# Performance work log

Hardware: AMD Instinct MI355X
Metric: run time of the kernel (lower is better)

## Reference

```python
import jax, jax.numpy as jnp
import numpy as np

V, A, N, C = 3, 4, 50000, 128


def setup_inputs() -> dict:
    key = jax.random.key(0)
    k1, k2, k3 = jax.random.split(key, 3)
    x = jax.random.normal(k1, (V, A, N, C), dtype=jnp.float32)
    # per-view Linear(in=C, out=C): weight [out,in], bias [out]
    W = jax.random.normal(k2, (V, C, C), dtype=jnp.float32) / np.sqrt(C)
    b = jax.random.normal(k3, (V, C), dtype=jnp.float32) * 0.01
    return {"x": x, "W": W, "b": b}


def reference(x, W, b):
    # per-view linear: out[v,a,n,d] = x[v,a,n,c] @ W[v,d,c]^T + b[v,d]
    out = jnp.einsum('vanc,vdc->vand', x, W) + b[:, None, None, :]
    # view summary: mean over nodes -> [V, A, C]
    s = x.mean(axis=2)
    # attention scores: s . out per node -> [V, A, N]
    scores = jnp.einsum('vac,vanc->van', s, out)
    # tanh then softmax across views (dim 0)
    w = jax.nn.softmax(jnp.tanh(scores), axis=0)
    # weighted combine of views -> [A, N, C]
    return jnp.einsum('van,vanc->anc', w, x)
```

## Files before the change

### kernel.cpp

```cpp
#include <hip/hip_runtime.h>
#include <hip/hip_bf16.h>

#define V 3
#define A 4
#define NN 50000
#define C 128
#define C4 32
#define CHUNKS 128
#define ROWS_PER ((NN + CHUNKS - 1) / CHUNKS)
#define VA (V * A)

typedef float nf4 __attribute__((ext_vector_type(4)));

__device__ __forceinline__ float dot4(float4 a, float4 b) {
    return a.x * b.x + a.y * b.y + a.z * b.z + a.w * b.w;
}

__device__ __forceinline__ float fast_tanh(float x) {
    float ax = fminf(fabsf(x), 15.f);
    float e  = __expf(2.f * ax);
    float r  = (e - 1.f) * __frcp_rn(e + 1.f);
    return copysignf(r, x);
}

__global__ void k_colsum(const float* __restrict__ x, float* __restrict__ part) {
    const int va    = blockIdx.y;
    const int chunk = blockIdx.x;
    const int n0 = chunk * ROWS_PER;
    const int n1 = (n0 + ROWS_PER < NN) ? (n0 + ROWS_PER) : NN;

    const int lane4 = threadIdx.x & 31;
    const int rowIn = threadIdx.x >> 5;

    const float4* xp = (const float4*)(x + (size_t)va * NN * C);
    float4 acc = {0.f, 0.f, 0.f, 0.f};
    #pragma unroll 4
    for (int n = n0 + rowIn; n < n1; n += 8) {
        float4 v = xp[(size_t)n * C4 + lane4];
        acc.x += v.x; acc.y += v.y; acc.z += v.z; acc.w += v.w;
    }

    __shared__ float4 red[256];
    red[threadIdx.x] = acc;
    __syncthreads();
    if (threadIdx.x < 32) {
        float4 t = red[threadIdx.x];
        #pragma unroll
        for (int r = 1; r < 8; r++) {
            float4 o = red[threadIdx.x + 32 * r];
            t.x += o.x; t.y += o.y; t.z += o.z; t.w += o.w;
        }
        ((float4*)part)[((size_t)chunk * VA + va) * C4 + lane4] = t;
    }
}

__global__ void k_tvec(const float* __restrict__ part, const float* __restrict__ W,
                       const float* __restrict__ b, float* __restrict__ t,
                       float* __restrict__ c0) {
    const int va   = blockIdx.x;
    const int v    = va / A;
    const int c    = threadIdx.x & 127;
    const int half = threadIdx.x >> 7;

    float acc = 0.f;
    #pragma unroll 8
    for (int ch = half * 64; ch < half * 64 + 64; ch++)
        acc += part[((size_t)ch * VA + va) * C + c];

    __shared__ float red[2][C];
    __shared__ float sb[C];
    __shared__ float pb[C];
    red[half][c] = acc;
    __syncthreads();
    if (threadIdx.x < C)
        sb[c] = (red[0][c] + red[1][c]) * (1.0f / (float)NN);
    __syncthreads();

    const float* Wv = W + (size_t)v * C * C;
    float t_acc = 0.f;
    #pragma unroll 8
    for (int d = half * 64; d < half * 64 + 64; d++)
        t_acc += sb[d] * Wv[d * C + c];
    red[half][c] = t_acc;
    __syncthreads();
    if (threadIdx.x < C) {
        t[va * C + c] = red[0][c] + red[1][c];
        pb[c] = sb[c] * b[v * C + c];
    }
    __syncthreads();
    #pragma unroll
    for (int s = 64; s > 0; s >>= 1) {
        if (threadIdx.x < s) pb[threadIdx.x] += pb[threadIdx.x + s];
        __syncthreads();
    }
    if (threadIdx.x == 0) c0[va] = pb[0];
}

__global__ void k_main(const float* __restrict__ x, const float* __restrict__ t,
                       const float* __restrict__ c0, float* __restrict__ out) {
    const int lane = threadIdx.x & 31;
    const int grp  = threadIdx.x >> 5;
    const int a    = blockIdx.y;
    const int n0   = (NN - 16) - blockIdx.x * 16 + grp * 2;

    const size_t vstride = (size_t)A * NN * C4;
    const float4* xp = (const float4*)x;
    const size_t baseA = ((size_t)a * NN + n0) * C4 + lane;
    const size_t baseB = baseA + C4;

    float4 xa0 = xp[baseA];
    float4 xa1 = xp[baseA + vstride];
    float4 xa2 = xp[baseA + 2 * vstride];
    float4 xb0 = xp[baseB];
    float4 xb1 = xp[baseB + vstride];
    float4 xb2 = xp[baseB + 2 * vstride];

    const float4* tp = (const float4*)t;
    float4 t0 = tp[(0 * A + a) * C4 + lane];
    float4 t1 = tp[(1 * A + a) * C4 + lane];
    float4 t2 = tp[(2 * A + a) * C4 + lane];

    float da0 = dot4(xa0, t0), da1 = dot4(xa1, t1), da2 = dot4(xa2, t2);
    float db0 = dot4(xb0, t0), db1 = dot4(xb1, t1), db2 = dot4(xb2, t2);

    #pragma unroll
    for (int off = 16; off > 0; off >>= 1) {
        da0 += __shfl_xor(da0, off, 32);
        da1 += __shfl_xor(da1, off, 32);
        da2 += __shfl_xor(da2, off, 32);
        db0 += __shfl_xor(db0, off, 32);
        db1 += __shfl_xor(db1, off, 32);
        db2 += __shfl_xor(db2, off, 32);
    }

    const float cc0 = c0[0 * A + a], cc1 = c0[1 * A + a], cc2 = c0[2 * A + a];

    float sa0 = fast_tanh(da0 + cc0);
    float sa1 = fast_tanh(da1 + cc1);
    float sa2 = fast_tanh(da2 + cc2);
    float ma  = fmaxf(sa0, fmaxf(sa1, sa2));
    float ea0 = __expf(sa0 - ma), ea1 = __expf(sa1 - ma), ea2 = __expf(sa2 - ma);
    float inva = __frcp_rn(ea0 + ea1 + ea2);
    float wa0 = ea0 * inva, wa1 = ea1 * inva, wa2 = ea2 * inva;

    float sb0 = fast_tanh(db0 + cc0);
    float sb1 = fast_tanh(db1 + cc1);
    float sb2 = fast_tanh(db2 + cc2);
    float mb  = fmaxf(sb0, fmaxf(sb1, sb2));
    float eb0 = __expf(sb0 - mb), eb1 = __expf(sb1 - mb), eb2 = __expf(sb2 - mb);
    float invb = __frcp_rn(eb0 + eb1 + eb2);
    float wb0 = eb0 * invb, wb1 = eb1 * invb, wb2 = eb2 * invb;

    nf4 oa, ob;
    oa.x = wa0 * xa0.x + wa1 * xa1.x + wa2 * xa2.x;
    oa.y = wa0 * xa0.y + wa1 * xa1.y + wa2 * xa2.y;
    oa.z = wa0 * xa0.z + wa1 * xa1.z + wa2 * xa2.z;
    oa.w = wa0 * xa0.w + wa1 * xa1.w + wa2 * xa2.w;
    ob.x = wb0 * xb0.x + wb1 * xb1.x + wb2 * xb2.x;
    ob.y = wb0 * xb0.y + wb1 * xb1.y + wb2 * xb2.y;
    ob.z = wb0 * xb0.z + wb1 * xb1.z + wb2 * xb2.z;
    ob.w = wb0 * xb0.w + wb1 * xb1.w + wb2 * xb2.w;

    nf4* op = (nf4*)out;
    const size_t obase = ((size_t)a * NN + n0) * C4 + lane;
    __builtin_nontemporal_store(oa, op + obase);
    __builtin_nontemporal_store(ob, op + obase + C4);
}

extern "C" void kernel_launch(void* const* d_in, const int* in_sizes, int n_in,
                              void* d_out, int out_size, void* d_ws, size_t ws_size,
                              hipStream_t stream) {
    const float* x = (const float*)d_in[0];
    const float* W = (const float*)d_in[1];
    const float* b = (const float*)d_in[2];
    float* out = (float*)d_out;

    float* part = (float*)d_ws;
    float* t    = part + (size_t)CHUNKS * VA * C;
    float* c0   = t + VA * C;

    k_colsum<<<dim3(CHUNKS, VA), 256, 0, stream>>>(x, part);
    k_tvec<<<VA, 256, 0, stream>>>(part, W, b, t, c0);
    k_main<<<dim3(NN / 16, A), 256, 0, stream>>>(x, t, c0, out);
}
```

Baseline: 490.2 us.

## Fuse three kernels into one persistent cooperative kernel with grid syncs

Merges the column-sum, summary/weight-vector and main combine kernels into a single cooperative persistent kernel separated by grid-wide barriers. Blocks loop over tasks and tiles, and the main phase loads the per-view t vectors and bias constants once per block instead of once per tile. The column-sum chunk count is doubled to spread work over the persistent grid. It removes launch gaps and tail effects between kernels. The cost is two grid syncs, the tvec phase running on only 12 blocks while the rest of the grid waits, and a fallback path if the cooperative launch fails.

Result: slower. 885.8 us (+80.7%).

```diff
diff --git a/kernel.cpp b/kernel.cpp
--- a/kernel.cpp
+++ b/kernel.cpp
@@ -1,14 +1,19 @@
 #include <hip/hip_runtime.h>
-#include <hip/hip_bf16.h>
+#include <hip/hip_cooperative_groups.h>
+
+namespace cg = cooperative_groups;
 
 #define V 3
 #define A 4
 #define NN 50000
 #define C 128
 #define C4 32
-#define CHUNKS 128
+#define CHUNKS 256
 #define ROWS_PER ((NN + CHUNKS - 1) / CHUNKS)
 #define VA (V * A)
+#define NTASKS (CHUNKS * VA)
+#define TILES (NN / 16)
+#define NBLK 1024
 
 typedef float nf4 __attribute__((ext_vector_type(4)));
 
@@ -23,9 +28,10 @@
     return copysignf(r, x);
 }
 
-__global__ void k_colsum(const float* __restrict__ x, float* __restrict__ part) {
-    const int va    = blockIdx.y;
-    const int chunk = blockIdx.x;
+__device__ __forceinline__ void colsum_task(const float* __restrict__ x,
+                                            float* __restrict__ part, int task) {
+    const int va    = task % VA;
+    const int chunk = task / VA;
     const int n0 = chunk * ROWS_PER;
     const int n1 = (n0 + ROWS_PER < NN) ? (n0 + ROWS_PER) : NN;
 
@@ -40,40 +46,42 @@
         acc.x += v.x; acc.y += v.y; acc.z += v.z; acc.w += v.w;
     }
 
-    __shared__ float4 red[256];
-    red[threadIdx.x] = acc;
+    __shared__ float4 redA[256];
+    redA[threadIdx.x] = acc;
     __syncthreads();
     if (threadIdx.x < 32) {
-        float4 t = red[threadIdx.x];
+        float4 t = redA[threadIdx.x];
         #pragma unroll
         for (int r = 1; r < 8; r++) {
-            float4 o = red[threadIdx.x + 32 * r];
+            float4 o = redA[threadIdx.x + 32 * r];
             t.x += o.x; t.y += o.y; t.z += o.z; t.w += o.w;
         }
         ((float4*)part)[((size_t)chunk * VA + va) * C4 + lane4] = t;
     }
-}
-
-__global__ void k_tvec(const float* __restrict__ part, const float* __restrict__ W,
-                       const float* __restrict__ b, float* __restrict__ t,
-                       float* __restrict__ c0) {
-    const int va   = blockIdx.x;
+    __syncthreads();
+}
+
+__device__ __forceinline__ void tvec_task(const float* __restrict__ part,
+                                          const float* __restrict__ W,
+                                          const float* __restrict__ b,
+                                          float* __restrict__ t,
+                                          float* __restrict__ c0, int va) {
     const int v    = va / A;
     const int c    = threadIdx.x & 127;
     const int half = threadIdx.x >> 7;
 
     float acc = 0.f;
     #pragma unroll 8
-    for (int ch = half * 64; ch < half * 64 + 64; ch++)
+    for (int ch = half * (CHUNKS / 2); ch < half * (CHUNKS / 2) + (CHUNKS / 2); ch++)
         acc += part[((size_t)ch * VA + va) * C + c];
 
-    __shared__ float red[2][C];
+    __shared__ float redB[2][C];
     __shared__ float sb[C];
     __shared__ float pb[C];
-    red[half][c] = acc;
+    redB[half][c] = acc;
     __syncthreads();
     if (threadIdx.x < C)
-        sb[c] = (red[0][c] + red[1][c]) * (1.0f / (float)NN);
+        sb[c] = (redB[0][c] + redB[1][c]) * (1.0f / (float)NN);
     __syncthreads();
 
     const float* Wv = W + (size_t)v * C * C;
@@ -81,10 +89,10 @@
     #pragma unroll 8
     for (int d = half * 64; d < half * 64 + 64; d++)
         t_acc += sb[d] * Wv[d * C + c];
-    red[half][c] = t_acc;
+    redB[half][c] = t_acc;
     __syncthreads();
     if (threadIdx.x < C) {
-        t[va * C + c] = red[0][c] + red[1][c];
+        t[va * C + c] = redB[0][c] + redB[1][c];
         pb[c] = sb[c] * b[v * C + c];
     }
     __syncthreads();
@@ -96,12 +104,13 @@
     if (threadIdx.x == 0) c0[va] = pb[0];
 }
 
-__global__ void k_main(const float* __restrict__ x, const float* __restrict__ t,
-                       const float* __restrict__ c0, float* __restrict__ out) {
+__device__ __forceinline__ void main_tile(const float* __restrict__ x,
+                                          float* __restrict__ out, int a, int tile,
+                                          float4 t0, float4 t1, float4 t2,
+                                          float cc0, float cc1, float cc2) {
     const int lane = threadIdx.x & 31;
     const int grp  = threadIdx.x >> 5;
-    const int a    = blockIdx.y;
-    const int n0   = (NN - 16) - blockIdx.x * 16 + grp * 2;
+    const int n0   = (NN - 16) - tile * 16 + grp * 2;
 
     const size_t vstride = (size_t)A * NN * C4;
     const float4* xp = (const float4*)x;
@@ -114,11 +123,6 @@
     float4 xb0 = xp[baseB];
     float4 xb1 = xp[baseB + vstride];
     float4 xb2 = xp[baseB + 2 * vstride];
-
-    const float4* tp = (const float4*)t;
-    float4 t0 = tp[(0 * A + a) * C4 + lane];
-    float4 t1 = tp[(1 * A + a) * C4 + lane];
-    float4 t2 = tp[(2 * A + a) * C4 + lane];
 
     float da0 = dot4(xa0, t0), da1 = dot4(xa1, t1), da2 = dot4(xa2, t2);
     float db0 = dot4(xb0, t0), db1 = dot4(xb1, t1), db2 = dot4(xb2, t2);
@@ -132,8 +136,6 @@
         db1 += __shfl_xor(db1, off, 32);
         db2 += __shfl_xor(db2, off, 32);
     }
-
-    const float cc0 = c0[0 * A + a], cc1 = c0[1 * A + a], cc2 = c0[2 * A + a];
 
     float sa0 = fast_tanh(da0 + cc0);
     float sa1 = fast_tanh(da1 + cc1);
@@ -167,6 +169,72 @@
     __builtin_nontemporal_store(ob, op + obase + C4);
 }
 
+__device__ __forceinline__ void phaseA(const float* __restrict__ x,
+                                       float* __restrict__ part) {
+    for (int task = blockIdx.x; task < NTASKS; task += gridDim.x)
+        colsum_task(x, part, task);
+}
+
+__device__ __forceinline__ void phaseC(const float* __restrict__ x,
+                                       const float* __restrict__ t,
+                                       const float* __restrict__ c0,
+                                       float* __restrict__ out) {
+    const int a     = blockIdx.x & 3;
+    const int bslot = blockIdx.x >> 2;
+    const int astr  = gridDim.x >> 2;
+    const int lane  = threadIdx.x & 31;
+
+    const float4* tp = (const float4*)t;
+    const float4 t0 = tp[(0 * A + a) * C4 + lane];
+    const float4 t1 = tp[(1 * A + a) * C4 + lane];
+    const float4 t2 = tp[(2 * A + a) * C4 + lane];
+    const float cc0 = c0[0 * A + a];
+    const float cc1 = c0[1 * A + a];
+    const float cc2 = c0[2 * A + a];
+
+    for (int tile = bslot; tile < TILES; tile += astr)
+        main_tile(x, out, a, tile, t0, t1, t2, cc0, cc1, cc2);
+}
+
+__global__ __launch_bounds__(256, 4) void k_fused(const float* __restrict__ x,
+                                                  const float* __restrict__ W,
+                                                  const float* __restrict__ b,
+                                                  float* __restrict__ out,
+                                                  float* __restrict__ ws) {
+    float* part = ws;
+    float* t    = ws + (size_t)CHUNKS * VA * C;
+    float* c0   = t + VA * C;
+
+    phaseA(x, part);
+    __threadfence();
+    cg::this_grid().sync();
+
+    if (blockIdx.x < VA)
+        tvec_task(part, W, b, t, c0, blockIdx.x);
+    __threadfence();
+    cg::this_grid().sync();
+
+    phaseC(x, t, c0, out);
+}
+
+__global__ __launch_bounds__(256, 4) void k_colsum2(const float* __restrict__ x,
+                                                    float* __restrict__ part) {
+    phaseA(x, part);
+}
+
+__global__ void k_tvec2(const float* __restrict__ part, const float* __restrict__ W,
+                        const float* __restrict__ b, float* __restrict__ t,
+                        float* __restrict__ c0) {
+    if (blockIdx.x < VA) tvec_task(part, W, b, t, c0, blockIdx.x);
+}
+
+__global__ __launch_bounds__(256, 4) void k_main2(const float* __restrict__ x,
+                                                  const float* __restrict__ t,
+                                                  const float* __restrict__ c0,
+                                                  float* __restrict__ out) {
+    phaseC(x, t, c0, out);
+}
+
 extern "C" void kernel_launch(void* const* d_in, const int* in_sizes, int n_in,
                               void* d_out, int out_size, void* d_ws, size_t ws_size,
                               hipStream_t stream) {
@@ -174,12 +242,36 @@
     const float* W = (const float*)d_in[1];
     const float* b = (const float*)d_in[2];
     float* out = (float*)d_out;
-
-    float* part = (float*)d_ws;
-    float* t    = part + (size_t)CHUNKS * VA * C;
-    float* c0   = t + VA * C;
-
-    k_colsum<<<dim3(CHUNKS, VA), 256, 0, stream>>>(x, part);
-    k_tvec<<<VA, 256, 0, stream>>>(part, W, b, t, c0);
-    k_main<<<dim3(NN / 16, A), 256, 0, stream>>>(x, t, c0, out);
-}
+    float* ws  = (float*)d_ws;
+
+    static int coopGrid = -1;
+    if (coopGrid < 0) {
+        int dev = 0;
+        (void)hipGetDevice(&dev);
+        int numCU = 0;
+        (void)hipDeviceGetAttribute(&numCU, hipDeviceAttributeMultiprocessorCount, dev);
+        if (numCU <= 0) numCU = 256;
+        int maxBlk = 0;
+        if (hipOccupancyMaxActiveBlocksPerMultiprocessor(&maxBlk, k_fused, 256, 0) != hipSuccess ||
+            maxBlk < 1)
+            maxBlk = 1;
+        long g = (long)numCU * (long)maxBlk;
+        if (g > NBLK) g = NBLK;
+        g &= ~3L;
+        if (g < 16) g = 16;
+        coopGrid = (int)g;
+    }
+
+    void* args[] = {(void*)&x, (void*)&W, (void*)&b, (void*)&out, (void*)&ws};
+    hipError_t err = hipLaunchCooperativeKernel((const void*)k_fused, dim3(coopGrid),
+                                                dim3(256), args, 0, stream);
+    if (err != hipSuccess) {
+        (void)hipGetLastError();
+        float* part = ws;
+        float* t    = part + (size_t)CHUNKS * VA * C;
+        float* c0   = t + VA * C;
+        k_colsum2<<<dim3(NBLK), 256, 0, stream>>>(x, part);
+        k_tvec2<<<dim3(VA), 256, 0, stream>>>(part, W, b, t, c0);
+        k_main2<<<dim3(NBLK), 256, 0, stream>>>(x, t, c0, out);
+    }
+}
```
